# Performance work log

Hardware: AMD Instinct MI355X
Metric: run time of the kernel (lower is better)

## Reference

```python
import jax, jax.numpy as jnp
import numpy as np

N_EMBD = 1024
N_HEAD = 16
HEAD_SIZE = N_EMBD // N_HEAD


def setup_inputs() -> dict:
    key = jax.random.key(0)
    k_x, k_w, k_b = jax.random.split(key, 3)
    B, T, C = 2, 2048, N_EMBD
    x = jax.random.normal(k_x, (B, T, C), dtype=jnp.float32)
    # Linear(n_embd, 3*n_embd): weight [C, 3C] (applied as x @ W), bias [3C]
    w_qkv = jax.random.normal(k_w, (C, 3 * C), dtype=jnp.float32) * (1.0 / np.sqrt(C))
    b_qkv = jax.random.normal(k_b, (3 * C,), dtype=jnp.float32) * 0.02
    return {"x": x, "w_qkv": w_qkv, "b_qkv": b_qkv}


def reference(x, w_qkv, b_qkv):
    B, T, C = x.shape
    H, D = N_HEAD, HEAD_SIZE
    qkv = x @ w_qkv + b_qkv                      # [B, T, 3C]
    q, k, v = jnp.split(qkv, 3, axis=-1)         # each [B, T, C]
    # [B, T, C] -> [B, H, T, D]
    q = q.reshape(B, T, H, D).transpose(0, 2, 1, 3)
    k = k.reshape(B, T, H, D).transpose(0, 2, 1, 3)
    v = v.reshape(B, T, H, D).transpose(0, 2, 1, 3)
    scores = jnp.einsum('bhqd,bhkd->bhqk', q, k) / jnp.sqrt(jnp.float32(D))
    causal = jnp.tril(jnp.ones((T, T), dtype=bool))  # allow j <= i
    scores = jnp.where(causal[None, None, :, :], scores, -jnp.inf)
    weights = jax.nn.softmax(scores, axis=-1)    # [B, H, T, T]
    out = jnp.einsum('bhqk,bhkd->bhqd', weights, v)
    out = out.transpose(0, 2, 1, 3).reshape(B, T, C)
    return out
```

## Files before the change

kernel.cpp:

```cpp
#include <hip/hip_runtime.h>
#include <hip/hip_bf16.h>


#define CDIM  1024
#define C3    3072
#define HS    64
#define TLEN  2048
#define KVT   128
#define KSTR  72
#define VSTR  136
#define SCL   0.1803368801111204f

typedef __attribute__((ext_vector_type(8))) short bf16x8;
typedef __attribute__((ext_vector_type(4))) float f32x4;
typedef __attribute__((ext_vector_type(4))) unsigned short u16x4;

__device__ __forceinline__ unsigned short f2b(float f) {
    unsigned u = __float_as_uint(f);
    unsigned r = (u + 0x7FFFu + ((u >> 16) & 1u)) >> 16;
    return (unsigned short)r;
}
__device__ __forceinline__ float b2f(unsigned short u) {
    return __uint_as_float(((unsigned)u) << 16);
}
__device__ __forceinline__ float fexp2(float x) {
    return __builtin_amdgcn_exp2f(x);
}
__device__ __forceinline__ unsigned pkbf(float a, float b) {
    float2 f; f.x = a; f.y = b;
    __hip_bfloat162 h = __float22bfloat162_rn(f);
    union { __hip_bfloat162 h2; unsigned u; } c;
    c.h2 = h;
    return c.u;
}
__device__ __forceinline__ void gl_lds16(const unsigned short* g, unsigned short* l) {
    __builtin_amdgcn_global_load_lds((const __attribute__((address_space(1))) void*)g,
                                     (__attribute__((address_space(3))) void*)l, 16, 0, 0);
}
__device__ __forceinline__ int detect_bf(const void* bias, int lane) {
    unsigned w = ((const unsigned*)bias)[lane];
    unsigned e = (w >> 7) & 0xFF;
    unsigned long long m = __ballot(e >= 100 && e <= 135);
    return __popcll(m) >= 48;
}

__global__ __launch_bounds__(256) void k_prep(const void* __restrict__ w,
                                              const void* __restrict__ x,
                                              const void* __restrict__ bias,
                                              unsigned short* __restrict__ wt,
                                              unsigned short* __restrict__ xb) {
    __shared__ unsigned short tile[64 * 66];
    int t = threadIdx.x;
    int isbf = detect_bf(bias, t & 63);
    int bid = blockIdx.x;

    if (bid < 768) {
        int n0 = (bid % 48) * 64;
        int k0 = (bid / 48) * 64;
        for (int i = 0; i < 16; ++i) {
            int idx = t + i * 256;
            int r = idx >> 6, c = idx & 63;
            unsigned short v;
            if (isbf) v = ((const unsigned short*)w)[(k0 + r) * C3 + n0 + c];
            else      v = f2b(((const float*)w)[(k0 + r) * C3 + n0 + c]);
            tile[r * 66 + c] = v;
        }
        __syncthreads();
        for (int i = 0; i < 16; ++i) {
            int idx = t + i * 256;
            int r = idx >> 6, c = idx & 63;
            wt[(n0 + r) * CDIM + k0 + c] = tile[c * 66 + r];
        }
    }
    if (!isbf) {
        const float* s = (const float*)x;
        unsigned* d = (unsigned*)xb;
        int base = bid * 1024;
        for (int j = t; j < 1024; j += 256) {
            int idx = base + j;
            float a = s[2 * idx], b = s[2 * idx + 1];
            d[idx] = (unsigned)f2b(a) | ((unsigned)f2b(b) << 16);
        }
    }
}

__global__ __launch_bounds__(256, 3) void k_gemm_qkv(const void* __restrict__ xraw,
                                                     const unsigned short* __restrict__ xb,
                                                     const void* __restrict__ biasraw,
                                                     const unsigned short* __restrict__ Bt,
                                                     unsigned short* __restrict__ qk,
                                                     unsigned short* __restrict__ vtg) {
    __shared__ __align__(16) unsigned short As[128 * 64];
    __shared__ __align__(16) unsigned short Bs[128 * 64];
    int tid  = threadIdx.x;
    int lane = tid & 63, wv = tid >> 6;
    int quad = lane >> 4, l16 = lane & 15;
    int isbf = detect_bf(biasraw, lane);
    const unsigned short* A = isbf ? (const unsigned short*)xraw : xb;

    int m0 = blockIdx.y * 128, n0 = blockIdx.x * 128;
    int wm = (wv >> 1) * 64, wn = (wv & 1) * 64;

    f32x4 acc[4][4] = {};

    int srow = wv * 8 + (lane >> 3);
    int kcg8 = (((lane & 7) ^ (lane >> 3)) * 8);
    const unsigned short* Ag = A  + (m0 + srow) * CDIM + kcg8;
    const unsigned short* Bg = Bt + (n0 + srow) * CDIM + kcg8;
    unsigned short* lA = &As[srow * 64 + (lane & 7) * 8];
    unsigned short* lB = &Bs[srow * 64 + (lane & 7) * 8];

    for (int k0 = 0; k0 < CDIM; k0 += 64) {
        __syncthreads();
        for (int j = 0; j < 4; ++j) {
            gl_lds16(Ag + j * (32 * CDIM), lA + j * (32 * 64));
            gl_lds16(Bg + j * (32 * CDIM), lB + j * (32 * 64));
        }
        Ag += 64; Bg += 64;
        __syncthreads();

        for (int kk = 0; kk < 2; ++kk) {
            int sw = (l16 & 7);
            bf16x8 af[4], bfr[4];
            for (int mt = 0; mt < 4; ++mt)
                af[mt] = *(const bf16x8*)&As[(wm + mt * 16 + l16) * 64 + (((kk * 4 + quad) ^ sw) * 8)];
            for (int nt = 0; nt < 4; ++nt)
                bfr[nt] = *(const bf16x8*)&Bs[(wn + nt * 16 + l16) * 64 + (((kk * 4 + quad) ^ sw) * 8)];
            for (int mt = 0; mt < 4; ++mt)
                for (int nt = 0; nt < 4; ++nt)
                    acc[mt][nt] = __builtin_amdgcn_mfma_f32_16x16x32_bf16(af[mt], bfr[nt], acc[mt][nt], 0, 0, 0);
        }
    }

    if (n0 < 2048) {
        for (int mt = 0; mt < 4; ++mt) {
            int row = m0 + wm + mt * 16 + quad * 4;
            for (int nt = 0; nt < 4; ++nt) {
                int col = n0 + wn + nt * 16 + l16;
                float bv = isbf ? b2f(((const unsigned short*)biasraw)[col])
                                : ((const float*)biasraw)[col];
                for (int i = 0; i < 4; ++i)
                    qk[(row + i) * 2048 + col] = f2b(acc[mt][nt][i] + bv);
            }
        }
    } else {
        for (int mt = 0; mt < 4; ++mt) {
            int row = m0 + wm + mt * 16 + quad * 4;
            int t = row & 2047, b = row >> 11;
            for (int nt = 0; nt < 4; ++nt) {
                int col = n0 + wn + nt * 16 + l16;
                float bv = isbf ? b2f(((const unsigned short*)biasraw)[col])
                                : ((const float*)biasraw)[col];
                int hh = (col - 2048) >> 6, d = (col - 2048) & 63;
                u16x4 pk;
                for (int i = 0; i < 4; ++i) pk[i] = f2b(acc[mt][nt][i] + bv);
                *(u16x4*)&vtg[((b * 16 + hh) * 64 + d) * TLEN + t] = pk;
            }
        }
    }
}

__global__ __launch_bounds__(256, 2) void k_attn(const unsigned short* __restrict__ qk,
                                                 const unsigned short* __restrict__ vtg,
                                                 const void* __restrict__ biasraw,
                                                 void* __restrict__ outv) {
    __shared__ __align__(16) unsigned short Ks[128 * KSTR];
    __shared__ __align__(16) unsigned short Vt[64 * VSTR];
    __shared__ __align__(16) unsigned short Pt[4][32 * VSTR];

    int tid  = threadIdx.x;
    int lane = tid & 63, wv = tid >> 6;
    int quad = lane >> 4, l16 = lane & 15;
    int isbf = detect_bf(biasraw, lane);
    int bh = blockIdx.x;
    int a  = blockIdx.y;
    int b = bh >> 4, h = bh & 15;
    int rowbase = b * TLEN;
    unsigned short* Pw = Pt[wv];

    int qtA = 4 * a + wv;
    int qtB = 127 - 4 * a - wv;
    int qA0 = qtA * 16, qB0 = qtB * 16;
    int tripsA = ((4 * a + wv) >> 3) + 1;
    int T      = ((127 - 4 * a - wv) >> 3) + 1;

    bf16x8 qfA[2], qfB[2];
    for (int kh = 0; kh < 2; ++kh) {
        qfA[kh] = *(const bf16x8*)&qk[(rowbase + qA0 + l16) * 2048 + h * HS + kh * 32 + quad * 8];
        qfB[kh] = *(const bf16x8*)&qk[(rowbase + qB0 + l16) * 2048 + h * HS + kh * 32 + quad * 8];
    }

    f32x4 oA[4] = {}, oB[4] = {};
    float lsA = 0.f, lsB = 0.f;

    int sr  = tid >> 3;
    int sc8 = (tid & 7) * 8;

    for (int t = 0; t < T; ++t) {
        int kv0 = t * KVT;
        bool actA = (t < tripsA);
        const unsigned short* kg = qk  + (rowbase + kv0 + sr) * 2048 + CDIM + h * HS + sc8;
        const unsigned short* vg = vtg + (bh * 64 + sr) * TLEN + kv0 + sc8;
        uint4 kr0 = *(const uint4*)kg;
        uint4 kr1 = *(const uint4*)(kg + 32 * 2048);
        uint4 kr2 = *(const uint4*)(kg + 64 * 2048);
        uint4 kr3 = *(const uint4*)(kg + 96 * 2048);
        uint4 vr0 = *(const uint4*)vg;
        uint4 vr1 = *(const uint4*)(vg + 64);
        uint4 vr2 = *(const uint4*)(vg + 32 * TLEN);
        uint4 vr3 = *(const uint4*)(vg + 32 * TLEN + 64);
        __syncthreads();
        *(uint4*)&Ks[sr * KSTR + sc8]        = kr0;
        *(uint4*)&Ks[(sr + 32) * KSTR + sc8] = kr1;
        *(uint4*)&Ks[(sr + 64) * KSTR + sc8] = kr2;
        *(uint4*)&Ks[(sr + 96) * KSTR + sc8] = kr3;
        *(uint4*)&Vt[sr * VSTR + sc8]        = vr0;
        *(uint4*)&Vt[sr * VSTR + sc8 + 64]   = vr1;
        *(uint4*)&Vt[(sr + 32) * VSTR + sc8]      = vr2;
        *(uint4*)&Vt[(sr + 32) * VSTR + sc8 + 64] = vr3;
        __syncthreads();

        f32x4 sA[8], sB[8];
        for (int nt = 0; nt < 8; ++nt) {
            bf16x8 kf0 = *(const bf16x8*)&Ks[(nt * 16 + l16) * KSTR + quad * 8];
            bf16x8 kf1 = *(const bf16x8*)&Ks[(nt * 16 + l16) * KSTR + 32 + quad * 8];
            f32x4 zB = {};
            zB = __builtin_amdgcn_mfma_f32_16x16x32_bf16(kf0, qfB[0], zB, 0, 0, 0);
            zB = __builtin_amdgcn_mfma_f32_16x16x32_bf16(kf1, qfB[1], zB, 0, 0, 0);
            sB[nt] = zB;
            if (actA) {
                f32x4 zA = {};
                zA = __builtin_amdgcn_mfma_f32_16x16x32_bf16(kf0, qfA[0], zA, 0, 0, 0);
                zA = __builtin_amdgcn_mfma_f32_16x16x32_bf16(kf1, qfA[1], zA, 0, 0, 0);
                sA[nt] = zA;
            }
        }

        {
            bool dmB = (t == T - 1);
            int q = qB0 + l16;
            float psum = 0.f;
            for (int nt = 0; nt < 8; ++nt) {
                float p[4];
                for (int i = 0; i < 4; ++i) {
                    float arg = fminf(fmaf(sB[nt][i], SCL, -12.0f), 30.0f);
                    if (dmB) {
                        int kv = kv0 + nt * 16 + quad * 4 + i;
                        if (kv > q) arg = -1e30f;
                    }
                    p[i] = fexp2(arg);
                    psum += p[i];
                }
                uint2 pk;
                pk.x = pkbf(p[0], p[1]);
                pk.y = pkbf(p[2], p[3]);
                *(uint2*)&Pw[(16 + l16) * VSTR + nt * 16 + quad * 4] = pk;
            }
            lsB += psum;
        }
        if (actA) {
            bool dmA = (t == tripsA - 1);
            int q = qA0 + l16;
            float psum = 0.f;
            for (int nt = 0; nt < 8; ++nt) {
                float p[4];
                for (int i = 0; i < 4; ++i) {
                    float arg = fminf(fmaf(sA[nt][i], SCL, -12.0f), 30.0f);
                    if (dmA) {
                        int kv = kv0 + nt * 16 + quad * 4 + i;
                        if (kv > q) arg = -1e30f;
                    }
                    p[i] = fexp2(arg);
                    psum += p[i];
                }
                uint2 pk;
                pk.x = pkbf(p[0], p[1]);
                pk.y = pkbf(p[2], p[3]);
                *(uint2*)&Pw[l16 * VSTR + nt * 16 + quad * 4] = pk;
            }
            lsA += psum;
        }

        for (int kh = 0; kh < 4; ++kh) {
            bf16x8 bpB = *(const bf16x8*)&Pw[(16 + l16) * VSTR + kh * 32 + quad * 8];
            if (actA) {
                bf16x8 bpA = *(const bf16x8*)&Pw[l16 * VSTR + kh * 32 + quad * 8];
                for (int dt = 0; dt < 4; ++dt) {
                    bf16x8 av = *(const bf16x8*)&Vt[(dt * 16 + l16) * VSTR + kh * 32 + quad * 8];
                    oB[dt] = __builtin_amdgcn_mfma_f32_16x16x32_bf16(av, bpB, oB[dt], 0, 0, 0);
                    oA[dt] = __builtin_amdgcn_mfma_f32_16x16x32_bf16(av, bpA, oA[dt], 0, 0, 0);
                }
            } else {
                for (int dt = 0; dt < 4; ++dt) {
                    bf16x8 av = *(const bf16x8*)&Vt[(dt * 16 + l16) * VSTR + kh * 32 + quad * 8];
                    oB[dt] = __builtin_amdgcn_mfma_f32_16x16x32_bf16(av, bpB, oB[dt], 0, 0, 0);
                }
            }
        }
    }

    for (int qt = 0; qt < 2; ++qt) {
        float l = qt ? lsB : lsA;
        const f32x4* oo = qt ? oB : oA;
        int q0 = qt ? qB0 : qA0;
        l += __shfl_xor(l, 16);
        l += __shfl_xor(l, 32);
        float inv = 1.0f / l;
        int q = q0 + l16;
        if (isbf) {
            unsigned short* out = (unsigned short*)outv;
            for (int dt = 0; dt < 4; ++dt) {
                u16x4 ov;
                for (int i = 0; i < 4; ++i) ov[i] = f2b(oo[dt][i] * inv);
                *(u16x4*)&out[(rowbase + q) * CDIM + h * HS + dt * 16 + quad * 4] = ov;
            }
        } else {
            float* out = (float*)outv;
            for (int dt = 0; dt < 4; ++dt) {
                float4 ov;
                ov.x = oo[dt][0] * inv; ov.y = oo[dt][1] * inv;
                ov.z = oo[dt][2] * inv; ov.w = oo[dt][3] * inv;
                *(float4*)&out[(rowbase + q) * CDIM + h * HS + dt * 16 + quad * 4] = ov;
            }
        }
    }
}

extern "C" void kernel_launch(void* const* d_in, const int* in_sizes, int n_in,
                              void* d_out, int out_size, void* d_ws, size_t ws_size,
                              hipStream_t stream) {
    const void* x    = d_in[0];
    const void* w    = d_in[1];
    const void* bias = d_in[2];

    char* ws = (char*)d_ws;
    unsigned short* xb  = (unsigned short*)ws;
    unsigned short* wt  = (unsigned short*)(ws + (8u  << 20));
    unsigned short* qk  = (unsigned short*)(ws + (16u << 20));
    unsigned short* vtg = (unsigned short*)(ws + (32u << 20));

    k_prep<<<2048, 256, 0, stream>>>(w, x, bias, wt, xb);
    k_gemm_qkv<<<dim3(24, 32), 256, 0, stream>>>(x, xb, bias, wt, qk, vtg);
    k_attn<<<dim3(32, 16), 256, 0, stream>>>(qk, vtg, bias, d_out);
}
```

Baseline: 155.8 us.

## Double-buffer K/V tiles, keep P in registers via permlane swaps, widen attention blocks

The attention kernel now runs 8 waves per block (512 threads) over half as many blocks. K/V tiles are double-buffered in LDS, and the next tile is prefetched into registers during compute, which removes one barrier per iteration. The softmax probabilities no longer round-trip through an LDS scratch buffer; they are rearranged into MFMA B-operand layout with v_permlane32/16_swap. It also raises wave priority around the PV MFMAs. The trade-off is more register pressure and larger LDS use at 512 threads, which may lower occupancy, and the permlane operand mapping has to be exactly right.

```diff
diff --git a/kernel.cpp b/kernel.cpp
--- a/kernel.cpp
+++ b/kernel.cpp
@@ -42,6 +42,27 @@
     unsigned e = (w >> 7) & 0xFF;
     unsigned long long m = __ballot(e >= 100 && e <= 135);
     return __popcll(m) >= 48;
+}
+
+__device__ __forceinline__ void plswap(unsigned x, unsigned& y0, unsigned& y1) {
+    unsigned aa = x, bb = x;
+    asm("v_permlane32_swap_b32 %0, %1" : "+v"(aa), "+v"(bb));
+    asm("v_permlane16_swap_b32 %0, %1" : "+v"(aa), "+v"(bb));
+    y0 = aa; y1 = bb;
+}
+__device__ __forceinline__ bf16x8 xfrag(unsigned x00, unsigned x01,
+                                        unsigned x10, unsigned x11, int qsel) {
+    unsigned y000, y100, y001, y101, y010, y110, y011, y111;
+    plswap(x00, y000, y100);
+    plswap(x01, y001, y101);
+    plswap(x10, y010, y110);
+    plswap(x11, y011, y111);
+    union { unsigned u[4]; bf16x8 v; } r;
+    r.u[0] = qsel ? y010 : y000;
+    r.u[1] = qsel ? y011 : y001;
+    r.u[2] = qsel ? y110 : y100;
+    r.u[3] = qsel ? y111 : y101;
+    return r.v;
 }
 
 __global__ __launch_bounds__(256) void k_prep(const void* __restrict__ w,
@@ -160,13 +181,12 @@
     }
 }
 
-__global__ __launch_bounds__(256, 2) void k_attn(const unsigned short* __restrict__ qk,
+__global__ __launch_bounds__(512, 2) void k_attn(const unsigned short* __restrict__ qk,
                                                  const unsigned short* __restrict__ vtg,
                                                  const void* __restrict__ biasraw,
                                                  void* __restrict__ outv) {
-    __shared__ __align__(16) unsigned short Ks[128 * KSTR];
-    __shared__ __align__(16) unsigned short Vt[64 * VSTR];
-    __shared__ __align__(16) unsigned short Pt[4][32 * VSTR];
+    __shared__ __align__(16) unsigned short Ks[2][128 * KSTR];
+    __shared__ __align__(16) unsigned short Vt[2][64 * VSTR];
 
     int tid  = threadIdx.x;
     int lane = tid & 63, wv = tid >> 6;
@@ -176,13 +196,12 @@
     int a  = blockIdx.y;
     int b = bh >> 4, h = bh & 15;
     int rowbase = b * TLEN;
-    unsigned short* Pw = Pt[wv];
-
-    int qtA = 4 * a + wv;
-    int qtB = 127 - 4 * a - wv;
+
+    int qtA = 8 * a + wv;
+    int qtB = 127 - qtA;
     int qA0 = qtA * 16, qB0 = qtB * 16;
-    int tripsA = ((4 * a + wv) >> 3) + 1;
-    int T      = ((127 - 4 * a - wv) >> 3) + 1;
+    int tripsA = a + 1;
+    int T      = 16 - a;
 
     bf16x8 qfA[2], qfB[2];
     for (int kh = 0; kh < 2; ++kh) {
@@ -193,37 +212,50 @@
     f32x4 oA[4] = {}, oB[4] = {};
     float lsA = 0.f, lsB = 0.f;
 
-    int sr  = tid >> 3;
-    int sc8 = (tid & 7) * 8;
+    int krow = tid >> 3;
+    int kc8  = (tid & 7) * 8;
+    int vrow = tid >> 4;
+    int vc8  = (tid & 15) * 8;
+    const unsigned short* kgB = qk  + (rowbase + krow) * 2048 + CDIM + h * HS + kc8;
+    const unsigned short* vgB = vtg + (bh * 64 + vrow) * TLEN + vc8;
+
+    {
+        uint4 k0 = *(const uint4*)kgB;
+        uint4 k1 = *(const uint4*)(kgB + 64 * 2048);
+        uint4 v0 = *(const uint4*)vgB;
+        uint4 v1 = *(const uint4*)(vgB + 32 * TLEN);
+        *(uint4*)&Ks[0][krow * KSTR + kc8]        = k0;
+        *(uint4*)&Ks[0][(krow + 64) * KSTR + kc8] = k1;
+        *(uint4*)&Vt[0][vrow * VSTR + vc8]        = v0;
+        *(uint4*)&Vt[0][(vrow + 32) * VSTR + vc8] = v1;
+    }
+    __syncthreads();
 
     for (int t = 0; t < T; ++t) {
+        int cur = t & 1;
+        const unsigned short* KsC = Ks[cur];
+        const unsigned short* VtC = Vt[cur];
+        bool actA = (t < tripsA);
+        bool dmA  = (t == tripsA - 1);
+        bool dmB  = (t == T - 1);
         int kv0 = t * KVT;
-        bool actA = (t < tripsA);
-        const unsigned short* kg = qk  + (rowbase + kv0 + sr) * 2048 + CDIM + h * HS + sc8;
-        const unsigned short* vg = vtg + (bh * 64 + sr) * TLEN + kv0 + sc8;
-        uint4 kr0 = *(const uint4*)kg;
-        uint4 kr1 = *(const uint4*)(kg + 32 * 2048);
-        uint4 kr2 = *(const uint4*)(kg + 64 * 2048);
-        uint4 kr3 = *(const uint4*)(kg + 96 * 2048);
-        uint4 vr0 = *(const uint4*)vg;
-        uint4 vr1 = *(const uint4*)(vg + 64);
-        uint4 vr2 = *(const uint4*)(vg + 32 * TLEN);
-        uint4 vr3 = *(const uint4*)(vg + 32 * TLEN + 64);
-        __syncthreads();
-        *(uint4*)&Ks[sr * KSTR + sc8]        = kr0;
-        *(uint4*)&Ks[(sr + 32) * KSTR + sc8] = kr1;
-        *(uint4*)&Ks[(sr + 64) * KSTR + sc8] = kr2;
-        *(uint4*)&Ks[(sr + 96) * KSTR + sc8] = kr3;
-        *(uint4*)&Vt[sr * VSTR + sc8]        = vr0;
-        *(uint4*)&Vt[sr * VSTR + sc8 + 64]   = vr1;
-        *(uint4*)&Vt[(sr + 32) * VSTR + sc8]      = vr2;
-        *(uint4*)&Vt[(sr + 32) * VSTR + sc8 + 64] = vr3;
-        __syncthreads();
-
-        f32x4 sA[8], sB[8];
+
+        uint4 kn0, kn1, vn0, vn1;
+        bool pf = (t + 1 < T);
+        if (pf) {
+            const unsigned short* kg = kgB + (t + 1) * KVT * 2048;
+            const unsigned short* vg = vgB + (t + 1) * KVT;
+            kn0 = *(const uint4*)kg;
+            kn1 = *(const uint4*)(kg + 64 * 2048);
+            vn0 = *(const uint4*)vg;
+            vn1 = *(const uint4*)(vg + 32 * TLEN);
+        }
+
+        f32x4 sB[8], sA[8];
+        #pragma unroll
         for (int nt = 0; nt < 8; ++nt) {
-            bf16x8 kf0 = *(const bf16x8*)&Ks[(nt * 16 + l16) * KSTR + quad * 8];
-            bf16x8 kf1 = *(const bf16x8*)&Ks[(nt * 16 + l16) * KSTR + 32 + quad * 8];
+            bf16x8 kf0 = *(const bf16x8*)&KsC[(nt * 16 + l16) * KSTR + quad * 8];
+            bf16x8 kf1 = *(const bf16x8*)&KsC[(nt * 16 + l16) * KSTR + 32 + quad * 8];
             f32x4 zB = {};
             zB = __builtin_amdgcn_mfma_f32_16x16x32_bf16(kf0, qfB[0], zB, 0, 0, 0);
             zB = __builtin_amdgcn_mfma_f32_16x16x32_bf16(kf1, qfB[1], zB, 0, 0, 0);
@@ -236,12 +268,14 @@
             }
         }
 
+        unsigned spB[8][2], spA[8][2];
         {
-            bool dmB = (t == T - 1);
             int q = qB0 + l16;
             float psum = 0.f;
+            #pragma unroll
             for (int nt = 0; nt < 8; ++nt) {
                 float p[4];
+                #pragma unroll
                 for (int i = 0; i < 4; ++i) {
                     float arg = fminf(fmaf(sB[nt][i], SCL, -12.0f), 30.0f);
                     if (dmB) {
@@ -251,19 +285,18 @@
                     p[i] = fexp2(arg);
                     psum += p[i];
                 }
-                uint2 pk;
-                pk.x = pkbf(p[0], p[1]);
-                pk.y = pkbf(p[2], p[3]);
-                *(uint2*)&Pw[(16 + l16) * VSTR + nt * 16 + quad * 4] = pk;
+                spB[nt][0] = pkbf(p[0], p[1]);
+                spB[nt][1] = pkbf(p[2], p[3]);
             }
             lsB += psum;
         }
         if (actA) {
-            bool dmA = (t == tripsA - 1);
             int q = qA0 + l16;
             float psum = 0.f;
+            #pragma unroll
             for (int nt = 0; nt < 8; ++nt) {
                 float p[4];
+                #pragma unroll
                 for (int i = 0; i < 4; ++i) {
                     float arg = fminf(fmaf(sA[nt][i], SCL, -12.0f), 30.0f);
                     if (dmA) {
@@ -273,30 +306,47 @@
                     p[i] = fexp2(arg);
                     psum += p[i];
                 }
-                uint2 pk;
-                pk.x = pkbf(p[0], p[1]);
-                pk.y = pkbf(p[2], p[3]);
-                *(uint2*)&Pw[l16 * VSTR + nt * 16 + quad * 4] = pk;
+                spA[nt][0] = pkbf(p[0], p[1]);
+                spA[nt][1] = pkbf(p[2], p[3]);
             }
             lsA += psum;
         }
 
-        for (int kh = 0; kh < 4; ++kh) {
-            bf16x8 bpB = *(const bf16x8*)&Pw[(16 + l16) * VSTR + kh * 32 + quad * 8];
+        int qsel = quad & 2;
+        #pragma unroll
+        for (int kq = 0; kq < 4; ++kq) {
+            bf16x8 fB = xfrag(spB[2 * kq][0], spB[2 * kq][1],
+                              spB[2 * kq + 1][0], spB[2 * kq + 1][1], qsel);
             if (actA) {
-                bf16x8 bpA = *(const bf16x8*)&Pw[l16 * VSTR + kh * 32 + quad * 8];
+                bf16x8 fA = xfrag(spA[2 * kq][0], spA[2 * kq][1],
+                                  spA[2 * kq + 1][0], spA[2 * kq + 1][1], qsel);
+                __builtin_amdgcn_s_setprio(1);
+                #pragma unroll
                 for (int dt = 0; dt < 4; ++dt) {
-                    bf16x8 av = *(const bf16x8*)&Vt[(dt * 16 + l16) * VSTR + kh * 32 + quad * 8];
-                    oB[dt] = __builtin_amdgcn_mfma_f32_16x16x32_bf16(av, bpB, oB[dt], 0, 0, 0);
-                    oA[dt] = __builtin_amdgcn_mfma_f32_16x16x32_bf16(av, bpA, oA[dt], 0, 0, 0);
+                    bf16x8 av = *(const bf16x8*)&VtC[(dt * 16 + l16) * VSTR + kq * 32 + quad * 8];
+                    oB[dt] = __builtin_amdgcn_mfma_f32_16x16x32_bf16(av, fB, oB[dt], 0, 0, 0);
+                    oA[dt] = __builtin_amdgcn_mfma_f32_16x16x32_bf16(av, fA, oA[dt], 0, 0, 0);
                 }
+                __builtin_amdgcn_s_setprio(0);
             } else {
+                __builtin_amdgcn_s_setprio(1);
+                #pragma unroll
                 for (int dt = 0; dt < 4; ++dt) {
-                    bf16x8 av = *(const bf16x8*)&Vt[(dt * 16 + l16) * VSTR + kh * 32 + quad * 8];
-                    oB[dt] = __builtin_amdgcn_mfma_f32_16x16x32_bf16(av, bpB, oB[dt], 0, 0, 0);
+                    bf16x8 av = *(const bf16x8*)&VtC[(dt * 16 + l16) * VSTR + kq * 32 + quad * 8];
+                    oB[dt] = __builtin_amdgcn_mfma_f32_16x16x32_bf16(av, fB, oB[dt], 0, 0, 0);
                 }
-            }
-        }
+                __builtin_amdgcn_s_setprio(0);
+            }
+        }
+
+        if (pf) {
+            int nxt = cur ^ 1;
+            *(uint4*)&Ks[nxt][krow * KSTR + kc8]        = kn0;
+            *(uint4*)&Ks[nxt][(krow + 64) * KSTR + kc8] = kn1;
+            *(uint4*)&Vt[nxt][vrow * VSTR + vc8]        = vn0;
+            *(uint4*)&Vt[nxt][(vrow + 32) * VSTR + vc8] = vn1;
+        }
+        __syncthreads();
     }
 
     for (int qt = 0; qt < 2; ++qt) {
@@ -341,5 +391,5 @@
 
     k_prep<<<2048, 256, 0, stream>>>(w, x, bias, wt, xb);
     k_gemm_qkv<<<dim3(24, 32), 256, 0, stream>>>(x, xb, bias, wt, qk, vtg);
-    k_attn<<<dim3(32, 16), 256, 0, stream>>>(qk, vtg, bias, d_out);
-}
+    k_attn<<<dim3(32, 8), 512, 0, stream>>>(qk, vtg, bias, d_out);
+}
```

Result: slower. 165.0 us (+5.9%).
